# Optimization experiments

Hardware: AMD Instinct MI355X
Metric: run time of the kernel (lower is better)

## Reference

```python
import jax, jax.numpy as jnp
import numpy as np

EMBED_DIM = 256
NUM_HEADS = 8
PROJ_DIM = EMBED_DIM // NUM_HEADS


def setup_inputs() -> dict:
    key = jax.random.key(0)
    ks = jax.random.split(key, 5)
    scale = 1.0 / np.sqrt(EMBED_DIM)
    inputs = jax.random.normal(ks[0], (2, 12, 12, 12, EMBED_DIM), dtype=jnp.float32)
    Wq = jax.random.normal(ks[1], (EMBED_DIM, EMBED_DIM), dtype=jnp.float32) * scale
    Wk = jax.random.normal(ks[2], (EMBED_DIM, EMBED_DIM), dtype=jnp.float32) * scale
    Wv = jax.random.normal(ks[3], (EMBED_DIM, EMBED_DIM), dtype=jnp.float32) * scale
    Wo = jax.random.normal(ks[4], (EMBED_DIM, EMBED_DIM), dtype=jnp.float32) * scale
    z = jnp.zeros((EMBED_DIM,), dtype=jnp.float32)
    return {"inputs": inputs, "Wq": Wq, "bq": z, "Wk": Wk, "bk": z,
            "Wv": Wv, "bv": z, "Wo": Wo, "bo": z}


def reference(inputs, Wq, bq, Wk, bk, Wv, bv, Wo, bo):
    B, h, w, d, E = inputs.shape
    S = h * w * d  # flattened spatial sequence
    x = inputs.reshape(B, S, E)
    # projections + head split: [B, S, E] -> [B, H, S, P]
    def split_heads(t):
        return t.reshape(B, S, NUM_HEADS, PROJ_DIM).transpose(0, 2, 1, 3)
    q = split_heads(x @ Wq + bq)
    k = split_heads(x @ Wk + bk)
    v = split_heads(x @ Wv + bv)
    # NOTE: original module does NOT scale by 1/sqrt(proj_dim)
    scores = jnp.einsum('bhsp,bhtp->bhst', q, k)  # [B, H, S, S]
    attn = jax.nn.softmax(scores, axis=-1)
    out = jnp.einsum('bhst,bhtp->bhsp', attn, v)  # [B, H, S, P]
    out = out.transpose(0, 2, 1, 3).reshape(B, h, w, d, E)
    return out @ Wo + bo
```

## Files before the change

kernel.cpp:

```cpp
#include <hip/hip_runtime.h>
#include <math.h>

#define EMBED 256
#define HEADS 8
#define PDIM  32
#define BATCH 2
#define SEQ   1728
#define NTOK  (BATCH*SEQ)
#define NE    (NTOK*EMBED)
#define KVB   128
#define NMAIN 13
#define TAIL0 1664
#define LOG2E 1.44269504088896f

typedef __attribute__((ext_vector_type(8))) __bf16 bf16x8;
typedef __attribute__((ext_vector_type(4))) float  f32x4;
typedef unsigned short ushort_t;
typedef unsigned int   uint_t;

static __device__ __forceinline__ unsigned short f2bf_rne(float f) {
    union { float f; unsigned u; } x; x.f = f;
    unsigned r = x.u + 0x7fffu + ((x.u >> 16) & 1u);
    return (unsigned short)(r >> 16);
}
union v8cast { uint4 u; bf16x8 v; };

static __device__ __forceinline__ void cvt8_hilo(const float f[8], bf16x8& hi, bf16x8& lo) {
    uint4 ph, pl;
    uint_t* phv = (uint_t*)&ph; uint_t* plv = (uint_t*)&pl;
    #pragma unroll
    for (int j = 0; j < 4; ++j) {
        const float f0 = f[2 * j], f1 = f[2 * j + 1];
        const uint_t u0 = __float_as_uint(f0) + 0x8000u;
        const uint_t u1 = __float_as_uint(f1) + 0x8000u;
        phv[j] = __builtin_amdgcn_perm(u1, u0, 0x07060302u);
        const float l0 = f0 - __uint_as_float(u0 & 0xFFFF0000u);
        const float l1 = f1 - __uint_as_float(u1 & 0xFFFF0000u);
        plv[j] = __builtin_amdgcn_perm(__float_as_uint(l1) + 0x8000u,
                                       __float_as_uint(l0) + 0x8000u, 0x07060302u);
    }
    v8cast ch; ch.u = ph; hi = ch.v;
    v8cast cl; cl.u = pl; lo = cl.v;
}

__global__ __launch_bounds__(64) void qkv_gemm_kernel(
    const float* __restrict__ x,
    const float* __restrict__ Wq, const float* __restrict__ bq,
    const float* __restrict__ Wk, const float* __restrict__ bk,
    const float* __restrict__ Wv, const float* __restrict__ bv,
    ushort_t* __restrict__ qo, ushort_t* __restrict__ ko, ushort_t* __restrict__ vt)
{
    const int lane = threadIdx.x, li = lane & 15, quad = lane >> 4;
    const int m0 = blockIdx.x * 32, n0 = blockIdx.y * 32, z = blockIdx.z;
    const float* __restrict__ W    = (z == 0) ? Wq : (z == 1) ? Wk : Wv;
    const float* __restrict__ bias = (z == 0) ? bq : (z == 1) ? bk : bv;

    const float* ap = x + (size_t)(m0 + li) * EMBED + quad * 8;

    f32x4 acc[2][2];
    #pragma unroll
    for (int mt = 0; mt < 2; ++mt)
        #pragma unroll
        for (int nt = 0; nt < 2; ++nt)
            acc[mt][nt] = (f32x4){0.f, 0.f, 0.f, 0.f};

    #pragma unroll 2
    for (int k0 = 0; k0 < EMBED; k0 += 32) {
        bf16x8 ah[2], al[2];
        #pragma unroll
        for (int mt = 0; mt < 2; ++mt) {
            float af[8];
            *(float4*)&af[0] = *(const float4*)(ap + (size_t)mt * 16 * EMBED + k0);
            *(float4*)&af[4] = *(const float4*)(ap + (size_t)mt * 16 * EMBED + k0 + 4);
            cvt8_hilo(af, ah[mt], al[mt]);
        }
        bf16x8 bh[2], bl[2];
        #pragma unroll
        for (int nt = 0; nt < 2; ++nt) {
            const int n = n0 + nt * 16 + li;
            const float* wp = W + (size_t)(k0 + quad * 8) * EMBED + n;
            float bf[8];
            #pragma unroll
            for (int jj = 0; jj < 8; ++jj) bf[jj] = wp[(size_t)jj * EMBED];
            cvt8_hilo(bf, bh[nt], bl[nt]);
        }
        #pragma unroll
        for (int mt = 0; mt < 2; ++mt)
            #pragma unroll
            for (int nt = 0; nt < 2; ++nt) {
                acc[mt][nt] = __builtin_amdgcn_mfma_f32_16x16x32_bf16(ah[mt], bh[nt], acc[mt][nt], 0, 0, 0);
                acc[mt][nt] = __builtin_amdgcn_mfma_f32_16x16x32_bf16(al[mt], bh[nt], acc[mt][nt], 0, 0, 0);
                acc[mt][nt] = __builtin_amdgcn_mfma_f32_16x16x32_bf16(ah[mt], bl[nt], acc[mt][nt], 0, 0, 0);
            }
    }

    const int b = m0 / SEQ;
    const int sbase = m0 - b * SEQ;

    if (z <= 1) {
        ushort_t* __restrict__ dst = z ? ko : qo;
        #pragma unroll
        for (int nt = 0; nt < 2; ++nt) {
            const int gcol = n0 + nt * 16 + li;
            const int h = gcol >> 5, p = gcol & 31;
            const float bb = bias[gcol];
            ushort_t* base = dst + ((size_t)(b * HEADS + h) * SEQ) * PDIM + p;
            #pragma unroll
            for (int mt = 0; mt < 2; ++mt)
                #pragma unroll
                for (int r = 0; r < 4; ++r) {
                    const int s = sbase + mt * 16 + quad * 4 + r;
                    base[(size_t)s * PDIM] = f2bf_rne(acc[mt][nt][r] + bb);
                }
        }
    } else {
        #pragma unroll
        for (int nt = 0; nt < 2; ++nt) {
            const int gcol = n0 + nt * 16 + li;
            const int h = gcol >> 5, p = gcol & 31;
            const float bb = bias[gcol];
            ushort_t* base = vt + ((size_t)(b * HEADS + h) * PDIM + p) * SEQ;
            #pragma unroll
            for (int mt = 0; mt < 2; ++mt) {
                const int s0 = sbase + mt * 16 + quad * 4;
                ushort4 w;
                w.x = f2bf_rne(acc[mt][nt][0] + bb);
                w.y = f2bf_rne(acc[mt][nt][1] + bb);
                w.z = f2bf_rne(acc[mt][nt][2] + bb);
                w.w = f2bf_rne(acc[mt][nt][3] + bb);
                *(ushort4*)&base[s0] = w;
            }
        }
    }
}

__global__ __launch_bounds__(256) void attn_kernel(
    const ushort_t* __restrict__ q, const ushort_t* __restrict__ k,
    const ushort_t* __restrict__ vt, ushort_t* __restrict__ aob)
{
    const int t    = threadIdx.x;
    const int lane = t & 63;
    const int w    = t >> 6;
    const int li   = lane & 15;
    const int quad = lane >> 4;
    const int bid = blockIdx.x;
    const int g = bid & 7, j = bid >> 3;
    const int bh = g * 2 + (j >= 27 ? 1 : 0);
    const int qt = (j >= 27) ? (j - 27) : j;
    const int b  = bh >> 3, h = bh & 7;
    const int q0 = qt * 64 + w * 16;

    const ushort_t* __restrict__ qb = q  + (size_t)bh * SEQ * PDIM;
    const ushort_t* __restrict__ kb = k  + (size_t)bh * SEQ * PDIM;
    const ushort_t* __restrict__ vb = vt + (size_t)bh * PDIM * SEQ;

    __shared__ ushort_t Ks[2][128][40];
    __shared__ ushort_t Vs[2][32][136];
    __shared__ ushort_t Ps[4][16][136];

    const bf16x8 qfrag = *(const bf16x8*)(qb + (size_t)(q0 + li) * PDIM + quad * 8);

    const int krow = t >> 1, kcol = (t & 1) * 16;
    const int vrow = t >> 3, vkey = (t & 7) * 16;
    const ushort_t* kgp = kb + (size_t)krow * PDIM + kcol;
    const ushort_t* vgp = vb + (size_t)vrow * SEQ + vkey;

    f32x4 o0 = {0.f, 0.f, 0.f, 0.f};
    f32x4 o1 = {0.f, 0.f, 0.f, 0.f};
    float m_run = -__builtin_inff(), l_run = 0.f;

    uint4 ka  = *(const uint4*)(kgp);
    uint4 kc  = *(const uint4*)(kgp + 8);
    uint4 va  = *(const uint4*)(vgp);
    uint4 vc  = *(const uint4*)(vgp + 8);

    for (int it = 0; it < NMAIN; ++it) {
        const int p = it & 1;
        *(uint4*)&Ks[p][krow][kcol]     = ka;
        *(uint4*)&Ks[p][krow][kcol + 8] = kc;
        *(uint4*)&Vs[p][vrow][vkey]     = va;
        *(uint4*)&Vs[p][vrow][vkey + 8] = vc;
        __syncthreads();
        if (it + 1 < NMAIN) {
            const size_t ko = (size_t)(it + 1) * KVB * PDIM;
            ka = *(const uint4*)(kgp + ko);
            kc = *(const uint4*)(kgp + ko + 8);
            va = *(const uint4*)(vgp + (it + 1) * KVB);
            vc = *(const uint4*)(vgp + (it + 1) * KVB + 8);
        } else {
            const ushort_t* kt_ = kb + (size_t)(TAIL0 + (krow & 63)) * PDIM + kcol;
            ka = *(const uint4*)(kt_);
            kc = *(const uint4*)(kt_ + 8);
            const ushort_t* vt_ = vb + (size_t)vrow * SEQ + TAIL0 + (vkey & 63);
            va = *(const uint4*)(vt_);
            vc = *(const uint4*)(vt_ + 8);
        }

        const f32x4 zero = {0.f, 0.f, 0.f, 0.f};
        f32x4 st[8];
        #pragma unroll
        for (int jt = 0; jt < 8; ++jt) {
            const bf16x8 kf = *(const bf16x8*)&Ks[p][jt * 16 + li][quad * 8];
            st[jt] = __builtin_amdgcn_mfma_f32_16x16x32_bf16(kf, qfrag, zero, 0, 0, 0);
        }

        float tm = st[0][0];
        #pragma unroll
        for (int jt = 0; jt < 8; ++jt)
            #pragma unroll
            for (int r = 0; r < 4; ++r) tm = fmaxf(tm, st[jt][r]);
        tm = fmaxf(tm, __shfl_xor(tm, 16));
        tm = fmaxf(tm, __shfl_xor(tm, 32));
        const float mnew  = fmaxf(m_run, tm);
        const float negml = -(mnew * LOG2E);

        float ps = 0.f;
        #pragma unroll
        for (int jt = 0; jt < 8; ++jt) {
            const float p0 = __builtin_amdgcn_exp2f(fmaf(st[jt][0], LOG2E, negml));
            const float p1 = __builtin_amdgcn_exp2f(fmaf(st[jt][1], LOG2E, negml));
            const float p2 = __builtin_amdgcn_exp2f(fmaf(st[jt][2], LOG2E, negml));
            const float p3 = __builtin_amdgcn_exp2f(fmaf(st[jt][3], LOG2E, negml));
            ps += (p0 + p1) + (p2 + p3);
            uint2 pw;
            pw.x = __builtin_amdgcn_perm(__float_as_uint(p1) + 0x8000u,
                                         __float_as_uint(p0) + 0x8000u, 0x07060302u);
            pw.y = __builtin_amdgcn_perm(__float_as_uint(p3) + 0x8000u,
                                         __float_as_uint(p2) + 0x8000u, 0x07060302u);
            *(uint2*)&Ps[w][li][16 * jt + 4 * quad] = pw;
        }
        ps += __shfl_xor(ps, 16);
        ps += __shfl_xor(ps, 32);

        const float alpha = __builtin_amdgcn_exp2f(fmaf(m_run, LOG2E, negml));
        l_run = fmaf(l_run, alpha, ps);
        m_run = mnew;

        float af[4];
        #pragma unroll
        for (int r = 0; r < 4; ++r) af[r] = __shfl(alpha, 4 * quad + r);
        #pragma unroll
        for (int r = 0; r < 4; ++r) { o0[r] *= af[r]; o1[r] *= af[r]; }

        #pragma unroll
        for (int c = 0; c < 4; ++c) {
            const bf16x8 pa  = *(const bf16x8*)&Ps[w][li][32 * c + 8 * quad];
            const bf16x8 vf0 = *(const bf16x8*)&Vs[p][li][32 * c + quad * 8];
            const bf16x8 vf1 = *(const bf16x8*)&Vs[p][16 + li][32 * c + quad * 8];
            o0 = __builtin_amdgcn_mfma_f32_16x16x32_bf16(pa, vf0, o0, 0, 0, 0);
            o1 = __builtin_amdgcn_mfma_f32_16x16x32_bf16(pa, vf1, o1, 0, 0, 0);
        }
    }

    {
        const int p = NMAIN & 1;
        *(uint4*)&Ks[p][krow][kcol]     = ka;
        *(uint4*)&Ks[p][krow][kcol + 8] = kc;
        *(uint4*)&Vs[p][vrow][vkey]     = va;
        *(uint4*)&Vs[p][vrow][vkey + 8] = vc;
        __syncthreads();

        const f32x4 zero = {0.f, 0.f, 0.f, 0.f};
        f32x4 st[4];
        #pragma unroll
        for (int jt = 0; jt < 4; ++jt) {
            const bf16x8 kf = *(const bf16x8*)&Ks[p][jt * 16 + li][quad * 8];
            st[jt] = __builtin_amdgcn_mfma_f32_16x16x32_bf16(kf, qfrag, zero, 0, 0, 0);
        }

        float tm = st[0][0];
        #pragma unroll
        for (int jt = 0; jt < 4; ++jt)
            #pragma unroll
            for (int r = 0; r < 4; ++r) tm = fmaxf(tm, st[jt][r]);
        tm = fmaxf(tm, __shfl_xor(tm, 16));
        tm = fmaxf(tm, __shfl_xor(tm, 32));
        const float mnew  = fmaxf(m_run, tm);
        const float negml = -(mnew * LOG2E);

        float ps = 0.f;
        #pragma unroll
        for (int jt = 0; jt < 4; ++jt) {
            const float p0 = __builtin_amdgcn_exp2f(fmaf(st[jt][0], LOG2E, negml));
            const float p1 = __builtin_amdgcn_exp2f(fmaf(st[jt][1], LOG2E, negml));
            const float p2 = __builtin_amdgcn_exp2f(fmaf(st[jt][2], LOG2E, negml));
            const float p3 = __builtin_amdgcn_exp2f(fmaf(st[jt][3], LOG2E, negml));
            ps += (p0 + p1) + (p2 + p3);
            uint2 pw;
            pw.x = __builtin_amdgcn_perm(__float_as_uint(p1) + 0x8000u,
                                         __float_as_uint(p0) + 0x8000u, 0x07060302u);
            pw.y = __builtin_amdgcn_perm(__float_as_uint(p3) + 0x8000u,
                                         __float_as_uint(p2) + 0x8000u, 0x07060302u);
            *(uint2*)&Ps[w][li][16 * jt + 4 * quad] = pw;
        }
        ps += __shfl_xor(ps, 16);
        ps += __shfl_xor(ps, 32);

        const float alpha = __builtin_amdgcn_exp2f(fmaf(m_run, LOG2E, negml));
        l_run = fmaf(l_run, alpha, ps);
        m_run = mnew;

        float af[4];
        #pragma unroll
        for (int r = 0; r < 4; ++r) af[r] = __shfl(alpha, 4 * quad + r);
        #pragma unroll
        for (int r = 0; r < 4; ++r) { o0[r] *= af[r]; o1[r] *= af[r]; }

        #pragma unroll
        for (int c = 0; c < 2; ++c) {
            const bf16x8 pa  = *(const bf16x8*)&Ps[w][li][32 * c + 8 * quad];
            const bf16x8 vf0 = *(const bf16x8*)&Vs[p][li][32 * c + quad * 8];
            const bf16x8 vf1 = *(const bf16x8*)&Vs[p][16 + li][32 * c + quad * 8];
            o0 = __builtin_amdgcn_mfma_f32_16x16x32_bf16(pa, vf0, o0, 0, 0, 0);
            o1 = __builtin_amdgcn_mfma_f32_16x16x32_bf16(pa, vf1, o1, 0, 0, 0);
        }
    }

    float linv[4];
    #pragma unroll
    for (int r = 0; r < 4; ++r) linv[r] = 1.0f / __shfl(l_run, 4 * quad + r);
    #pragma unroll
    for (int r = 0; r < 4; ++r) {
        const int s = q0 + 4 * quad + r;
        ushort_t* row = aob + ((size_t)(b * SEQ + s)) * EMBED + h * PDIM;
        row[li]      = f2bf_rne(o0[r] * linv[r]);
        row[16 + li] = f2bf_rne(o1[r] * linv[r]);
    }
}

__global__ __launch_bounds__(64) void out_gemm_kernel(
    const ushort_t* __restrict__ a, const float* __restrict__ Wo,
    const float* __restrict__ bo, float* __restrict__ out)
{
    const int lane = threadIdx.x, li = lane & 15, quad = lane >> 4;
    const int m0 = blockIdx.x * 32, n0 = blockIdx.y * 16;

    const ushort_t* aph = a + (size_t)(m0 + li) * EMBED + quad * 8;

    f32x4 acc[2];
    #pragma unroll
    for (int mt = 0; mt < 2; ++mt) acc[mt] = (f32x4){0.f, 0.f, 0.f, 0.f};

    #pragma unroll 2
    for (int k0 = 0; k0 < EMBED; k0 += 32) {
        bf16x8 ah[2];
        #pragma unroll
        for (int mt = 0; mt < 2; ++mt)
            ah[mt] = *(const bf16x8*)(aph + (size_t)mt * 16 * EMBED + k0);
        const float* wp = Wo + (size_t)(k0 + quad * 8) * EMBED + n0 + li;
        uint4 pb;
        uint_t* pbv = (uint_t*)&pb;
        #pragma unroll
        for (int j = 0; j < 4; ++j) {
            const uint_t u0 = __float_as_uint(wp[(size_t)(2 * j) * EMBED])     + 0x8000u;
            const uint_t u1 = __float_as_uint(wp[(size_t)(2 * j + 1) * EMBED]) + 0x8000u;
            pbv[j] = __builtin_amdgcn_perm(u1, u0, 0x07060302u);
        }
        v8cast cb; cb.u = pb;
        #pragma unroll
        for (int mt = 0; mt < 2; ++mt)
            acc[mt] = __builtin_amdgcn_mfma_f32_16x16x32_bf16(ah[mt], cb.v, acc[mt], 0, 0, 0);
    }

    const float bb = bo[n0 + li];
    #pragma unroll
    for (int mt = 0; mt < 2; ++mt)
        #pragma unroll
        for (int r = 0; r < 4; ++r) {
            const int row = m0 + mt * 16 + quad * 4 + r;
            out[(size_t)row * EMBED + n0 + li] = acc[mt][r] + bb;
        }
}

extern "C" void kernel_launch(void* const* d_in, const int* in_sizes, int n_in,
                              void* d_out, int out_size, void* d_ws, size_t ws_size,
                              hipStream_t stream)
{
    const float* x  = (const float*)d_in[0];
    const float* Wq = (const float*)d_in[1];
    const float* bq = (const float*)d_in[2];
    const float* Wk = (const float*)d_in[3];
    const float* bk = (const float*)d_in[4];
    const float* Wv = (const float*)d_in[5];
    const float* bv = (const float*)d_in[6];
    const float* Wo = (const float*)d_in[7];
    const float* bo = (const float*)d_in[8];
    float* out = (float*)d_out;

    ushort_t* ws  = (ushort_t*)d_ws;
    ushort_t* qb  = ws;
    ushort_t* kb  = qb + (size_t)NE;
    ushort_t* vt  = kb + (size_t)NE;
    ushort_t* aob = vt + (size_t)NE;

    qkv_gemm_kernel<<<dim3(NTOK / 32, 8, 3), 64, 0, stream>>>(
        x, Wq, bq, Wk, bk, Wv, bv, qb, kb, vt);
    attn_kernel<<<dim3(432), 256, 0, stream>>>(qb, kb, vt, aob);
    out_gemm_kernel<<<dim3(NTOK / 32, 16), 64, 0, stream>>>(aob, Wo, bo, out);
}
```

Baseline: 118.1 us.

## Tile QKV GEMM through double-buffered shared memory with 4-wave blocks

The QKV projection kernel moves from a single-wave 32x32 tile, where each wave loaded and split its own A/B fragments from global memory, to a 256-thread 64x64 tile. Each element is loaded and split to hi/lo bf16 once, stored into double-buffered LDS, and shared by four waves. The next k-slice is prefetched into registers while the current one is consumed. This cuts redundant global loads and hi/lo conversions, at the cost of LDS traffic, one barrier per k-step and fewer blocks in the grid.

```diff
diff --git a/kernel.cpp b/kernel.cpp
--- a/kernel.cpp
+++ b/kernel.cpp
@@ -43,19 +43,36 @@
     v8cast cl; cl.u = pl; lo = cl.v;
 }
 
-__global__ __launch_bounds__(64) void qkv_gemm_kernel(
+__global__ __launch_bounds__(256) void qkv_gemm_kernel(
     const float* __restrict__ x,
     const float* __restrict__ Wq, const float* __restrict__ bq,
     const float* __restrict__ Wk, const float* __restrict__ bk,
     const float* __restrict__ Wv, const float* __restrict__ bv,
     ushort_t* __restrict__ qo, ushort_t* __restrict__ ko, ushort_t* __restrict__ vt)
 {
-    const int lane = threadIdx.x, li = lane & 15, quad = lane >> 4;
-    const int m0 = blockIdx.x * 32, n0 = blockIdx.y * 32, z = blockIdx.z;
+    const int t = threadIdx.x;
+    const int lane = t & 63, li = lane & 15, quad = lane >> 4;
+    const int w = t >> 6, wm = w >> 1, wn = w & 1;
+    const int m0 = blockIdx.x * 64, n0 = blockIdx.y * 64, z = blockIdx.z;
     const float* __restrict__ W    = (z == 0) ? Wq : (z == 1) ? Wk : Wv;
     const float* __restrict__ bias = (z == 0) ? bq : (z == 1) ? bk : bv;
 
-    const float* ap = x + (size_t)(m0 + li) * EMBED + quad * 8;
+    __shared__ ushort_t Ah[2][64][40];
+    __shared__ ushort_t Al[2][64][40];
+    __shared__ ushort_t Bh[2][64][40];
+    __shared__ ushort_t Bl[2][64][40];
+
+    const int ar = t >> 2, ac = (t & 3) * 8;
+    const int bn = t & 63, bk8 = (t >> 6) * 8;
+
+    const float* agp = x + (size_t)(m0 + ar) * EMBED + ac;
+    const float* bgp = W + (size_t)bk8 * EMBED + n0 + bn;
+
+    float areg[8], breg[8];
+    *(float4*)&areg[0] = *(const float4*)(agp);
+    *(float4*)&areg[4] = *(const float4*)(agp + 4);
+    #pragma unroll
+    for (int j = 0; j < 8; ++j) breg[j] = bgp[(size_t)j * EMBED];
 
     f32x4 acc[2][2];
     #pragma unroll
@@ -64,44 +81,58 @@
         for (int nt = 0; nt < 2; ++nt)
             acc[mt][nt] = (f32x4){0.f, 0.f, 0.f, 0.f};
 
-    #pragma unroll 2
-    for (int k0 = 0; k0 < EMBED; k0 += 32) {
-        bf16x8 ah[2], al[2];
+    for (int ks = 0; ks < 8; ++ks) {
+        const int p = ks & 1;
+        {
+            bf16x8 h, l;
+            cvt8_hilo(areg, h, l);
+            v8cast ch; ch.v = h; *(uint4*)&Ah[p][ar][ac] = ch.u;
+            v8cast cl; cl.v = l; *(uint4*)&Al[p][ar][ac] = cl.u;
+        }
+        {
+            bf16x8 h, l;
+            cvt8_hilo(breg, h, l);
+            v8cast ch; ch.v = h; *(uint4*)&Bh[p][bn][bk8] = ch.u;
+            v8cast cl; cl.v = l; *(uint4*)&Bl[p][bn][bk8] = cl.u;
+        }
+        __syncthreads();
+        if (ks < 7) {
+            const int k1 = (ks + 1) * 32;
+            *(float4*)&areg[0] = *(const float4*)(agp + k1);
+            *(float4*)&areg[4] = *(const float4*)(agp + k1 + 4);
+            const float* bg = bgp + (size_t)k1 * EMBED;
+            #pragma unroll
+            for (int j = 0; j < 8; ++j) breg[j] = bg[(size_t)j * EMBED];
+        }
+        bf16x8 ah[2], al_[2], bh[2], bl_[2];
         #pragma unroll
         for (int mt = 0; mt < 2; ++mt) {
-            float af[8];
-            *(float4*)&af[0] = *(const float4*)(ap + (size_t)mt * 16 * EMBED + k0);
-            *(float4*)&af[4] = *(const float4*)(ap + (size_t)mt * 16 * EMBED + k0 + 4);
-            cvt8_hilo(af, ah[mt], al[mt]);
-        }
-        bf16x8 bh[2], bl[2];
+            ah[mt]  = *(const bf16x8*)&Ah[p][wm * 32 + mt * 16 + li][quad * 8];
+            al_[mt] = *(const bf16x8*)&Al[p][wm * 32 + mt * 16 + li][quad * 8];
+        }
         #pragma unroll
         for (int nt = 0; nt < 2; ++nt) {
-            const int n = n0 + nt * 16 + li;
-            const float* wp = W + (size_t)(k0 + quad * 8) * EMBED + n;
-            float bf[8];
-            #pragma unroll
-            for (int jj = 0; jj < 8; ++jj) bf[jj] = wp[(size_t)jj * EMBED];
-            cvt8_hilo(bf, bh[nt], bl[nt]);
+            bh[nt]  = *(const bf16x8*)&Bh[p][wn * 32 + nt * 16 + li][quad * 8];
+            bl_[nt] = *(const bf16x8*)&Bl[p][wn * 32 + nt * 16 + li][quad * 8];
         }
         #pragma unroll
         for (int mt = 0; mt < 2; ++mt)
             #pragma unroll
             for (int nt = 0; nt < 2; ++nt) {
-                acc[mt][nt] = __builtin_amdgcn_mfma_f32_16x16x32_bf16(ah[mt], bh[nt], acc[mt][nt], 0, 0, 0);
-                acc[mt][nt] = __builtin_amdgcn_mfma_f32_16x16x32_bf16(al[mt], bh[nt], acc[mt][nt], 0, 0, 0);
-                acc[mt][nt] = __builtin_amdgcn_mfma_f32_16x16x32_bf16(ah[mt], bl[nt], acc[mt][nt], 0, 0, 0);
+                acc[mt][nt] = __builtin_amdgcn_mfma_f32_16x16x32_bf16(ah[mt],  bh[nt],  acc[mt][nt], 0, 0, 0);
+                acc[mt][nt] = __builtin_amdgcn_mfma_f32_16x16x32_bf16(al_[mt], bh[nt],  acc[mt][nt], 0, 0, 0);
+                acc[mt][nt] = __builtin_amdgcn_mfma_f32_16x16x32_bf16(ah[mt],  bl_[nt], acc[mt][nt], 0, 0, 0);
             }
     }
 
     const int b = m0 / SEQ;
-    const int sbase = m0 - b * SEQ;
+    const int sbase = m0 - b * SEQ + wm * 32;
 
     if (z <= 1) {
         ushort_t* __restrict__ dst = z ? ko : qo;
         #pragma unroll
         for (int nt = 0; nt < 2; ++nt) {
-            const int gcol = n0 + nt * 16 + li;
+            const int gcol = n0 + wn * 32 + nt * 16 + li;
             const int h = gcol >> 5, p = gcol & 31;
             const float bb = bias[gcol];
             ushort_t* base = dst + ((size_t)(b * HEADS + h) * SEQ) * PDIM + p;
@@ -116,19 +147,19 @@
     } else {
         #pragma unroll
         for (int nt = 0; nt < 2; ++nt) {
-            const int gcol = n0 + nt * 16 + li;
+            const int gcol = n0 + wn * 32 + nt * 16 + li;
             const int h = gcol >> 5, p = gcol & 31;
             const float bb = bias[gcol];
             ushort_t* base = vt + ((size_t)(b * HEADS + h) * PDIM + p) * SEQ;
             #pragma unroll
             for (int mt = 0; mt < 2; ++mt) {
                 const int s0 = sbase + mt * 16 + quad * 4;
-                ushort4 w;
-                w.x = f2bf_rne(acc[mt][nt][0] + bb);
-                w.y = f2bf_rne(acc[mt][nt][1] + bb);
-                w.z = f2bf_rne(acc[mt][nt][2] + bb);
-                w.w = f2bf_rne(acc[mt][nt][3] + bb);
-                *(ushort4*)&base[s0] = w;
+                ushort4 wv4;
+                wv4.x = f2bf_rne(acc[mt][nt][0] + bb);
+                wv4.y = f2bf_rne(acc[mt][nt][1] + bb);
+                wv4.z = f2bf_rne(acc[mt][nt][2] + bb);
+                wv4.w = f2bf_rne(acc[mt][nt][3] + bb);
+                *(ushort4*)&base[s0] = wv4;
             }
         }
     }
@@ -393,7 +424,7 @@
     ushort_t* vt  = kb + (size_t)NE;
     ushort_t* aob = vt + (size_t)NE;
 
-    qkv_gemm_kernel<<<dim3(NTOK / 32, 8, 3), 64, 0, stream>>>(
+    qkv_gemm_kernel<<<dim3(NTOK / 64, EMBED / 64, 3), 256, 0, stream>>>(
         x, Wq, bq, Wk, bk, Wv, bv, qb, kb, vt);
     attn_kernel<<<dim3(432), 256, 0, stream>>>(qb, kb, vt, aob);
     out_gemm_kernel<<<dim3(NTOK / 32, 16), 64, 0, stream>>>(aob, Wo, bo, out);
```

Result: faster. 113.7 us (-3.8%).
